# Kernel optimization log

Hardware: AMD Instinct MI355X
Metric: run time of the kernel (lower is better)

The kernel has to match this reference:

```python
import jax, jax.numpy as jnp
import numpy as np

N, E, D, H, ED = 50000, 400000, 64, 4, 16
C = D  # out_channels per head (GATv2Conv(model_dim, model_dim, ...))


def setup_inputs() -> dict:
    key = jax.random.key(0)
    ks = jax.random.split(key, 24)
    sD = 1.0 / np.sqrt(D)
    sE = 1.0 / np.sqrt(ED)
    sC = 1.0 / np.sqrt(C)
    inp = {
        "h": jax.random.normal(ks[0], (N, D), jnp.float32),
        "edge_index": jax.random.randint(ks[1], (2, E), 0, N, dtype=jnp.int32),
        "edge_attr": jax.random.normal(ks[2], (E, ED), jnp.float32),
    }
    for i, name in enumerate(["g1", "g2"]):
        b = 3 + i * 9
        inp[f"{name}_Wl"] = jax.random.normal(ks[b], (D, H * C), jnp.float32) * sD
        inp[f"{name}_bl"] = jax.random.normal(ks[b + 1], (H * C,), jnp.float32) * 0.02
        inp[f"{name}_Wr"] = jax.random.normal(ks[b + 2], (D, H * C), jnp.float32) * sD
        inp[f"{name}_br"] = jax.random.normal(ks[b + 3], (H * C,), jnp.float32) * 0.02
        inp[f"{name}_We"] = jax.random.normal(ks[b + 4], (ED, H * C), jnp.float32) * sE
        inp[f"{name}_att"] = jax.random.normal(ks[b + 5], (H, C), jnp.float32) * sC
        inp[f"{name}_bias"] = jax.random.normal(ks[b + 6], (C,), jnp.float32) * 0.02
        inp[f"ln{i+1}_g"] = jnp.ones((D,), jnp.float32)
        inp[f"ln{i+1}_b"] = jnp.zeros((D,), jnp.float32)
    return inp


def _layer_norm(x, g, b):
    mu = jnp.mean(x, axis=-1, keepdims=True)
    var = jnp.mean((x - mu) ** 2, axis=-1, keepdims=True)
    return (x - mu) * jax.lax.rsqrt(var + 1e-5) * g + b


def _gatv2(h, src, dst, edge_attr, Wl, bl, Wr, br, We, att, bias):
    # PyG GATv2Conv, concat=False, negative_slope=0.2, aggregation at dst
    xl = (h @ Wl + bl).reshape(N, H, C)  # source transform
    xr = (h @ Wr + br).reshape(N, H, C)  # target transform
    ez = (edge_attr @ We).reshape(E, H, C)
    x = jax.nn.leaky_relu(xl[src] + xr[dst] + ez, negative_slope=0.2)  # [E,H,C]
    alpha = jnp.einsum('ehc,hc->eh', x, att)  # attention logits per edge/head
    amax = jax.ops.segment_max(alpha, dst, num_segments=N)
    amax = jnp.where(jnp.isfinite(amax), amax, 0.0)
    ex = jnp.exp(alpha - amax[dst])
    denom = jax.ops.segment_sum(ex, dst, num_segments=N)
    a = ex / (denom[dst] + 1e-16)  # segment softmax over incoming edges
    out = jax.ops.segment_sum(xl[src] * a[..., None], dst, num_segments=N)  # [N,H,C]
    return jnp.mean(out, axis=1) + bias  # concat=False -> head mean, then bias


def reference(h, edge_index, edge_attr,
              g1_Wl, g1_bl, g1_Wr, g1_br, g1_We, g1_att, g1_bias, ln1_g, ln1_b,
              g2_Wl, g2_bl, g2_Wr, g2_br, g2_We, g2_att, g2_bias, ln2_g, ln2_b):
    src, dst = edge_index[0], edge_index[1]
    identity = h
    x = _gatv2(h, src, dst, edge_attr, g1_Wl, g1_bl, g1_Wr, g1_br, g1_We, g1_att, g1_bias)
    x = jax.nn.gelu(_layer_norm(x, ln1_g, ln1_b), approximate=False)
    x = _gatv2(x, src, dst, edge_attr, g2_Wl, g2_bl, g2_Wr, g2_br, g2_We, g2_att, g2_bias)
    x = _layer_norm(x, ln2_g, ln2_b)
    return jax.nn.gelu(x + identity, approximate=False)
```

## Files before the change

### kernel.cpp

```cpp
#include <hip/hip_runtime.h>
#include <math.h>

#define NN  50000
#define EE  400000
#define DD  64
#define HH  4
#define HC  256
#define EDD 16

__device__ __forceinline__ float gelu_exact(float x) {
    return 0.5f * x * (1.0f + erff(x * 0.70710678118654752440f));
}
__device__ __forceinline__ float fast_exp(float x) {
    return __builtin_amdgcn_exp2f(x * 1.44269504088896340736f);
}

__global__ void fill_u32(unsigned* __restrict__ p, unsigned v, int n) {
    int i = blockIdx.x * blockDim.x + threadIdx.x;
    int s = gridDim.x * blockDim.x;
    for (; i < n; i += s) p[i] = v;
}

__global__ void hist_k(const int* __restrict__ ei, int* __restrict__ deg) {
    int e = blockIdx.x * 256 + threadIdx.x;
    if (e < EE) atomicAdd(&deg[ei[EE + e]], 1);
}
__global__ void scan1_k(const int* __restrict__ deg, int* __restrict__ rowptr,
                        int* __restrict__ bsum) {
    __shared__ int s[256];
    int t = threadIdx.x, i = blockIdx.x * 256 + t;
    int v = (i < NN) ? deg[i] : 0;
    s[t] = v; __syncthreads();
    for (int o = 1; o < 256; o <<= 1) {
        int u = (t >= o) ? s[t - o] : 0;
        __syncthreads();
        s[t] += u;
        __syncthreads();
    }
    if (i < NN) rowptr[i] = s[t] - v;
    if (t == 255) bsum[blockIdx.x] = s[255];
}
__global__ void scan2_k(int* __restrict__ bsum, int nb) {
    __shared__ int s[256];
    int t = threadIdx.x;
    int v = (t < nb) ? bsum[t] : 0;
    s[t] = v; __syncthreads();
    for (int o = 1; o < 256; o <<= 1) {
        int u = (t >= o) ? s[t - o] : 0;
        __syncthreads();
        s[t] += u;
        __syncthreads();
    }
    if (t < nb) bsum[t] = s[t] - v;
}
__global__ void scan3_k(int* __restrict__ rowptr, const int* __restrict__ bsum,
                        int* __restrict__ cursor) {
    int i = blockIdx.x * 256 + threadIdx.x;
    if (i < NN) {
        int r = rowptr[i] + bsum[blockIdx.x];
        rowptr[i] = r;
        cursor[i] = r;
    }
    if (i == 0) rowptr[NN] = EE;
}
__global__ void scatter_k(const int* __restrict__ ei, int* __restrict__ cursor,
                          const float* __restrict__ ea,
                          int* __restrict__ srcs, float* __restrict__ ea_s) {
    int e = blockIdx.x * 256 + threadIdx.x;
    if (e >= EE) return;
    int dst = ei[EE + e];
    int pos = atomicAdd(&cursor[dst], 1);
    srcs[pos] = ei[e];
    const float4* s4 = (const float4*)(ea + (long)e * EDD);
    float4* d4 = (float4*)(ea_s + (long)pos * EDD);
    d4[0] = s4[0]; d4[1] = s4[1]; d4[2] = s4[2]; d4[3] = s4[3];
}

__global__ void wrange_k(const int* __restrict__ rowptr, int* __restrict__ wstart,
                         int nw, int cpe) {
    int w = blockIdx.x * 256 + threadIdx.x;
    if (w > nw) return;
    if (w == nw) { wstart[nw] = NN; return; }
    const int lo = w * cpe;
    int l = 0, r = NN;
    while (l < r) { int m = (l + r) >> 1; if (rowptr[m] >= lo) r = m; else l = m + 1; }
    wstart[w] = l;
}

__global__ __launch_bounds__(256) void gemm_node_lr(
    const float* __restrict__ X,
    const float* __restrict__ Wl, const float* __restrict__ bl,
    const float* __restrict__ Wr, const float* __restrict__ br,
    float* __restrict__ Yl, float* __restrict__ Yr)
{
    __shared__ float xs[32][64];
    const int tid  = threadIdx.x;
    const int col  = tid;
    const int base = blockIdx.x * 32;

#pragma unroll
    for (int i = 0; i < 2; i++) {
        const int f   = tid + i * 256;
        const int r   = f >> 4;
        const int row = base + r;
        const int rr  = (row < NN) ? row : (NN - 1);
        const float4 v = *(const float4*)(X + (long)rr * 64 + ((f & 15) << 2));
        *(float4*)&xs[r][(f & 15) << 2] = v;
    }

    float wl[64], wr[64];
#pragma unroll
    for (int k = 0; k < 64; k++) wl[k] = Wl[k * 256 + col];
#pragma unroll
    for (int k = 0; k < 64; k++) wr[k] = Wr[k * 256 + col];
    const float bbl = bl[col];
    const float bbr = br[col];

    __syncthreads();

#pragma unroll 2
    for (int r = 0; r < 32; r++) {
        const int row = base + r;
        float l0 = 0.f, l1 = 0.f, l2 = 0.f, l3 = 0.f;
        float r0 = 0.f, r1 = 0.f, r2 = 0.f, r3 = 0.f;
#pragma unroll
        for (int k4 = 0; k4 < 16; k4++) {
            const float4 xv = *(const float4*)&xs[r][k4 << 2];
            l0 = fmaf(xv.x, wl[k4 * 4],     l0);
            l1 = fmaf(xv.y, wl[k4 * 4 + 1], l1);
            l2 = fmaf(xv.z, wl[k4 * 4 + 2], l2);
            l3 = fmaf(xv.w, wl[k4 * 4 + 3], l3);
            r0 = fmaf(xv.x, wr[k4 * 4],     r0);
            r1 = fmaf(xv.y, wr[k4 * 4 + 1], r1);
            r2 = fmaf(xv.z, wr[k4 * 4 + 2], r2);
            r3 = fmaf(xv.w, wr[k4 * 4 + 3], r3);
        }
        if (row < NN) {
            Yl[(long)row * 256 + col] = (l0 + l1) + (l2 + l3) + bbl;
            Yr[(long)row * 256 + col] = (r0 + r1) + (r2 + r3) + bbr;
        }
    }
}

__global__ __launch_bounds__(256, 4) void fused_edge_node_k(
    const int* __restrict__ wstart,
    const int* __restrict__ rowptr, const int* __restrict__ srcs,
    const float* __restrict__ ea_s,
    const float* __restrict__ We, const float* __restrict__ att,
    const float* __restrict__ xl, const float* __restrict__ xr,
    const float* __restrict__ bias, const float* __restrict__ lng,
    const float* __restrict__ lnb, const float* __restrict__ identity,
    float* __restrict__ x1out, float* __restrict__ outp, int mode)
{
    const int lane = threadIdx.x & 63;
    const int h    = lane >> 4;
    const int jj   = lane & 15;
    const int gc   = (h << 6) + (jj << 2);
    const int cb   = jj << 2;

    float wreg[EDD][4];
#pragma unroll
    for (int k = 0; k < EDD; k++) {
        const float4 w4 = *(const float4*)(We + k * HC + gc);
        wreg[k][0] = w4.x; wreg[k][1] = w4.y; wreg[k][2] = w4.z; wreg[k][3] = w4.w;
    }
#pragma unroll
    for (int k = 0; k < EDD; k++)
#pragma unroll
        for (int j = 0; j < 4; j++) asm volatile("" : "+v"(wreg[k][j]));

    const float4 a4 = *(const float4*)(att + gc);

    const int wid  = blockIdx.x * 4 + (threadIdx.x >> 6);
    const int nbeg = __builtin_amdgcn_readfirstlane(wstart[wid]);
    const int nend = __builtin_amdgcn_readfirstlane(wstart[wid + 1]);

    int p0v = rowptr[nbeg];
    int p1v = rowptr[nbeg + 1];
    int sAn = srcs[p0v];
    int sBn = srcs[p0v + 1];

    for (int n = nbeg; n < nend; n++) {
        const int p0 = __builtin_amdgcn_readfirstlane(p0v);
        const int p1 = __builtin_amdgcn_readfirstlane(p1v);
        p0v = p1;
        p1v = rowptr[(n + 2 <= NN) ? (n + 2) : NN];
        int sA = sAn, sB = sBn;
        sAn = srcs[p1];
        sBn = srcs[p1 + 1];

        const float4 xrv = *(const float4*)(xr + (long)n * HC + gc);

        float dsum = 0.f;
        float ac0 = 0.f, ac1 = 0.f, ac2 = 0.f, ac3 = 0.f;

        int p = p0;
        for (; p + 1 < p1; p += 2) {
            const int srcA = __builtin_amdgcn_readfirstlane(sA);
            const int srcB = __builtin_amdgcn_readfirstlane(sB);
            sA = srcs[p + 2];
            sB = srcs[p + 3];

            const float4 xlvA = *(const float4*)(xl + (long)srcA * HC + gc);
            const float4 xlvB = *(const float4*)(xl + (long)srcB * HC + gc);

            const float4* __restrict__ e4 = (const float4*)(ea_s + (long)p * EDD);
            float eavA[EDD], eavB[EDD];
            *(float4*)&eavA[0]  = e4[0];
            *(float4*)&eavA[4]  = e4[1];
            *(float4*)&eavA[8]  = e4[2];
            *(float4*)&eavA[12] = e4[3];
            *(float4*)&eavB[0]  = e4[4];
            *(float4*)&eavB[4]  = e4[5];
            *(float4*)&eavB[8]  = e4[6];
            *(float4*)&eavB[12] = e4[7];

            float eA0 = 0.f, eA1 = 0.f, eA2 = 0.f, eA3 = 0.f;
            float eB0 = 0.f, eB1 = 0.f, eB2 = 0.f, eB3 = 0.f;
#pragma unroll
            for (int k = 0; k < EDD; k++) {
                eA0 = fmaf(eavA[k], wreg[k][0], eA0);
                eA1 = fmaf(eavA[k], wreg[k][1], eA1);
                eA2 = fmaf(eavA[k], wreg[k][2], eA2);
                eA3 = fmaf(eavA[k], wreg[k][3], eA3);
                eB0 = fmaf(eavB[k], wreg[k][0], eB0);
                eB1 = fmaf(eavB[k], wreg[k][1], eB1);
                eB2 = fmaf(eavB[k], wreg[k][2], eB2);
                eB3 = fmaf(eavB[k], wreg[k][3], eB3);
            }
            float sA0 = xlvA.x + xrv.x + eA0;
            float sA1 = xlvA.y + xrv.y + eA1;
            float sA2 = xlvA.z + xrv.z + eA2;
            float sA3 = xlvA.w + xrv.w + eA3;
            float sB0 = xlvB.x + xrv.x + eB0;
            float sB1 = xlvB.y + xrv.y + eB1;
            float sB2 = xlvB.z + xrv.z + eB2;
            float sB3 = xlvB.w + xrv.w + eB3;
            sA0 = (sA0 > 0.f) ? sA0 : 0.2f * sA0;
            sA1 = (sA1 > 0.f) ? sA1 : 0.2f * sA1;
            sA2 = (sA2 > 0.f) ? sA2 : 0.2f * sA2;
            sA3 = (sA3 > 0.f) ? sA3 : 0.2f * sA3;
            sB0 = (sB0 > 0.f) ? sB0 : 0.2f * sB0;
            sB1 = (sB1 > 0.f) ? sB1 : 0.2f * sB1;
            sB2 = (sB2 > 0.f) ? sB2 : 0.2f * sB2;
            sB3 = (sB3 > 0.f) ? sB3 : 0.2f * sB3;
            float pA = fmaf(sA0, a4.x, fmaf(sA1, a4.y, fmaf(sA2, a4.z, sA3 * a4.w)));
            float pB = fmaf(sB0, a4.x, fmaf(sB1, a4.y, fmaf(sB2, a4.z, sB3 * a4.w)));
            pA += __shfl_xor(pA, 1, 64);
            pB += __shfl_xor(pB, 1, 64);
            pA += __shfl_xor(pA, 2, 64);
            pB += __shfl_xor(pB, 2, 64);
            pA += __shfl_xor(pA, 4, 64);
            pB += __shfl_xor(pB, 4, 64);
            pA += __shfl_xor(pA, 8, 64);
            pB += __shfl_xor(pB, 8, 64);

            const float wA = fast_exp(pA);
            const float wB = fast_exp(pB);
            dsum += (wA + wB);
            ac0 = fmaf(wA, xlvA.x, ac0);
            ac1 = fmaf(wA, xlvA.y, ac1);
            ac2 = fmaf(wA, xlvA.z, ac2);
            ac3 = fmaf(wA, xlvA.w, ac3);
            ac0 = fmaf(wB, xlvB.x, ac0);
            ac1 = fmaf(wB, xlvB.y, ac1);
            ac2 = fmaf(wB, xlvB.z, ac2);
            ac3 = fmaf(wB, xlvB.w, ac3);
        }

        if (p < p1) {
            const int src = __builtin_amdgcn_readfirstlane(sA);
            const float4 xlv = *(const float4*)(xl + (long)src * HC + gc);
            const float4* __restrict__ e4 = (const float4*)(ea_s + (long)p * EDD);
            float eav[EDD];
            *(float4*)&eav[0]  = e4[0];
            *(float4*)&eav[4]  = e4[1];
            *(float4*)&eav[8]  = e4[2];
            *(float4*)&eav[12] = e4[3];
            float ez0 = 0.f, ez1 = 0.f, ez2 = 0.f, ez3 = 0.f;
#pragma unroll
            for (int k = 0; k < EDD; k++) {
                ez0 = fmaf(eav[k], wreg[k][0], ez0);
                ez1 = fmaf(eav[k], wreg[k][1], ez1);
                ez2 = fmaf(eav[k], wreg[k][2], ez2);
                ez3 = fmaf(eav[k], wreg[k][3], ez3);
            }
            float s0 = xlv.x + xrv.x + ez0;
            float s1 = xlv.y + xrv.y + ez1;
            float s2 = xlv.z + xrv.z + ez2;
            float s3 = xlv.w + xrv.w + ez3;
            s0 = (s0 > 0.f) ? s0 : 0.2f * s0;
            s1 = (s1 > 0.f) ? s1 : 0.2f * s1;
            s2 = (s2 > 0.f) ? s2 : 0.2f * s2;
            s3 = (s3 > 0.f) ? s3 : 0.2f * s3;
            float part = fmaf(s0, a4.x, fmaf(s1, a4.y, fmaf(s2, a4.z, s3 * a4.w)));
            part += __shfl_xor(part, 1, 64);
            part += __shfl_xor(part, 2, 64);
            part += __shfl_xor(part, 4, 64);
            part += __shfl_xor(part, 8, 64);
            const float w = fast_exp(part);
            dsum += w;
            ac0 = fmaf(w, xlv.x, ac0);
            ac1 = fmaf(w, xlv.y, ac1);
            ac2 = fmaf(w, xlv.z, ac2);
            ac3 = fmaf(w, xlv.w, ac3);
        }

        const float inv = 1.0f / (dsum + 1e-16f);
        float v0 = ac0 * inv, v1 = ac1 * inv, v2 = ac2 * inv, v3 = ac3 * inv;

        v0 += __shfl_xor(v0, 16, 64); v0 += __shfl_xor(v0, 32, 64);
        v1 += __shfl_xor(v1, 16, 64); v1 += __shfl_xor(v1, 32, 64);
        v2 += __shfl_xor(v2, 16, 64); v2 += __shfl_xor(v2, 32, 64);
        v3 += __shfl_xor(v3, 16, 64); v3 += __shfl_xor(v3, 32, 64);

        if (lane < 16) {
            const float4 b4 = *(const float4*)(bias + cb);
            v0 = v0 * 0.25f + b4.x;
            v1 = v1 * 0.25f + b4.y;
            v2 = v2 * 0.25f + b4.z;
            v3 = v3 * 0.25f + b4.w;

            float s = (v0 + v1) + (v2 + v3);
            s += __shfl_xor(s, 1, 64); s += __shfl_xor(s, 2, 64);
            s += __shfl_xor(s, 4, 64); s += __shfl_xor(s, 8, 64);
            const float mu = s * (1.0f / 64.0f);
            const float d0 = v0 - mu, d1 = v1 - mu, d2 = v2 - mu, d3 = v3 - mu;
            float q = (d0 * d0 + d1 * d1) + (d2 * d2 + d3 * d3);
            q += __shfl_xor(q, 1, 64); q += __shfl_xor(q, 2, 64);
            q += __shfl_xor(q, 4, 64); q += __shfl_xor(q, 8, 64);
            const float rs = rsqrtf(q * (1.0f / 64.0f) + 1e-5f);

            const float4 g4 = *(const float4*)(lng + cb);
            const float4 c4 = *(const float4*)(lnb + cb);
            float y0 = d0 * rs * g4.x + c4.x;
            float y1 = d1 * rs * g4.y + c4.y;
            float y2 = d2 * rs * g4.z + c4.z;
            float y3 = d3 * rs * g4.w + c4.w;

            if (mode == 0) {
                float4 o;
                o.x = gelu_exact(y0); o.y = gelu_exact(y1);
                o.z = gelu_exact(y2); o.w = gelu_exact(y3);
                *(float4*)(x1out + (long)n * DD + cb) = o;
            } else {
                const float4 id = *(const float4*)(identity + (long)n * DD + cb);
                float4 o;
                o.x = gelu_exact(y0 + id.x); o.y = gelu_exact(y1 + id.y);
                o.z = gelu_exact(y2 + id.z); o.w = gelu_exact(y3 + id.w);
                *(float4*)(outp + (long)n * DD + cb) = o;
            }
        }
    }
}

extern "C" void kernel_launch(void* const* d_in, const int* in_sizes, int n_in,
                              void* d_out, int out_size, void* d_ws, size_t ws_size,
                              hipStream_t stream) {
    (void)in_sizes; (void)n_in; (void)out_size; (void)ws_size;

    const float* h     = (const float*)d_in[0];
    const int*   ei    = (const int*)d_in[1];
    const float* ea    = (const float*)d_in[2];
    const float* g1Wl  = (const float*)d_in[3];
    const float* g1bl  = (const float*)d_in[4];
    const float* g1Wr  = (const float*)d_in[5];
    const float* g1br  = (const float*)d_in[6];
    const float* g1We  = (const float*)d_in[7];
    const float* g1att = (const float*)d_in[8];
    const float* g1bias= (const float*)d_in[9];
    const float* ln1g  = (const float*)d_in[10];
    const float* ln1b  = (const float*)d_in[11];
    const float* g2Wl  = (const float*)d_in[12];
    const float* g2bl  = (const float*)d_in[13];
    const float* g2Wr  = (const float*)d_in[14];
    const float* g2br  = (const float*)d_in[15];
    const float* g2We  = (const float*)d_in[16];
    const float* g2att = (const float*)d_in[17];
    const float* g2bias= (const float*)d_in[18];
    const float* ln2g  = (const float*)d_in[19];
    const float* ln2b  = (const float*)d_in[20];

    float* out = (float*)d_out;

    const int FUSED_BLOCKS = 4096;
    const int NW  = FUSED_BLOCKS * 4;
    const int CPE = (EE + NW - 1) / NW;

    float* ws = (float*)d_ws;
    size_t o = 0;
    float* xl     = ws + o;         o += 12800000;
    float* xr     = ws + o;         o += 12800000;
    float* x1     = ws + o;         o += 3200000;
    int*   rowptr = (int*)(ws + o); o += 50004;
    int*   deg    = (int*)(ws + o); o += 50000;
    int*   cursor = (int*)(ws + o); o += 50000;
    int*   bsum   = (int*)(ws + o); o += 256;
    int*   srcs   = (int*)(ws + o); o += 400016;
    int*   wstart = (int*)(ws + o); o += NW + 8;
    float* ea_s   = ws + o;         o += 6400000;

    const int GEMM_BLOCKS  = (NN + 31) / 32;
    const int SCAN_BLOCKS  = (NN + 255) / 256;
    const int EDGE_BLOCKS  = (EE + 255) / 256;
    const int WR_BLOCKS    = (NW + 1 + 255) / 256;

    fill_u32<<<256, 256, 0, stream>>>((unsigned*)deg, 0u, NN);
    hist_k<<<EDGE_BLOCKS, 256, 0, stream>>>(ei, deg);
    scan1_k<<<SCAN_BLOCKS, 256, 0, stream>>>(deg, rowptr, bsum);
    scan2_k<<<1, 256, 0, stream>>>(bsum, SCAN_BLOCKS);
    scan3_k<<<SCAN_BLOCKS, 256, 0, stream>>>(rowptr, bsum, cursor);
    wrange_k<<<WR_BLOCKS, 256, 0, stream>>>(rowptr, wstart, NW, CPE);
    scatter_k<<<EDGE_BLOCKS, 256, 0, stream>>>(ei, cursor, ea, srcs, ea_s);

    gemm_node_lr<<<GEMM_BLOCKS, 256, 0, stream>>>(h, g1Wl, g1bl, g1Wr, g1br, xl, xr);
    fused_edge_node_k<<<FUSED_BLOCKS, 256, 0, stream>>>(wstart, rowptr, srcs, ea_s,
                                                        g1We, g1att, xl, xr,
                                                        g1bias, ln1g, ln1b,
                                                        h, x1, out, 0);

    gemm_node_lr<<<GEMM_BLOCKS, 256, 0, stream>>>(x1, g2Wl, g2bl, g2Wr, g2br, xl, xr);
    fused_edge_node_k<<<FUSED_BLOCKS, 256, 0, stream>>>(wstart, rowptr, srcs, ea_s,
                                                        g2We, g2att, xl, xr,
                                                        g2bias, ln2g, ln2b,
                                                        h, x1, out, 1);
}
```

Baseline: 495.5 us.

## Unroll edge loop by four with masked tail, DPP reductions, full-wave LayerNorm epilogue

The per-node edge loop now handles four edges per iteration and replaces the remainder path with -INFINITY masking. It pads srcs and ea_s so the over-read past the last edge stays in bounds. Head reductions use DPP row adds instead of cross-lane shuffles. The LayerNorm/GELU epilogue is spread over all 64 lanes, one channel each, instead of 16 lanes handling float4. The aim is more memory-level parallelism and fewer shuffle and idle-lane costs, at the price of wasted work on nodes whose in-degree is not a multiple of four and higher register pressure.

After: 522.3 us. 5.4% more time.

```diff
diff --git a/kernel.cpp b/kernel.cpp
--- a/kernel.cpp
+++ b/kernel.cpp
@@ -13,6 +13,19 @@
 }
 __device__ __forceinline__ float fast_exp(float x) {
     return __builtin_amdgcn_exp2f(x * 1.44269504088896340736f);
+}
+
+template <int CTRL>
+__device__ __forceinline__ float dpp_add(float x) {
+    const int t = __builtin_amdgcn_update_dpp(0, __float_as_int(x), CTRL, 0xF, 0xF, true);
+    return x + __int_as_float(t);
+}
+__device__ __forceinline__ float row_sum16(float x) {
+    x = dpp_add<0x128>(x);
+    x = dpp_add<0x124>(x);
+    x = dpp_add<0x122>(x);
+    x = dpp_add<0x121>(x);
+    return x;
 }
 
 __global__ void fill_u32(unsigned* __restrict__ p, unsigned v, int n) {
@@ -77,8 +90,9 @@
 }
 
 __global__ void wrange_k(const int* __restrict__ rowptr, int* __restrict__ wstart,
-                         int nw, int cpe) {
+                         int* __restrict__ srcs, int nw, int cpe) {
     int w = blockIdx.x * 256 + threadIdx.x;
+    if (blockIdx.x == 0 && threadIdx.x < 16) srcs[EE + threadIdx.x] = 0;
     if (w > nw) return;
     if (w == nw) { wstart[nw] = NN; return; }
     const int lo = w * cpe;
@@ -142,6 +156,28 @@
     }
 }
 
+__device__ __forceinline__ float edge_part(const float ev[EDD], const float wreg[EDD][4],
+                                           const float4 xlv, const float4 xrv,
+                                           const float4 a4) {
+    float e0 = 0.f, e1 = 0.f, e2 = 0.f, e3 = 0.f;
+#pragma unroll
+    for (int k = 0; k < EDD; k++) {
+        e0 = fmaf(ev[k], wreg[k][0], e0);
+        e1 = fmaf(ev[k], wreg[k][1], e1);
+        e2 = fmaf(ev[k], wreg[k][2], e2);
+        e3 = fmaf(ev[k], wreg[k][3], e3);
+    }
+    float s0 = xlv.x + xrv.x + e0;
+    float s1 = xlv.y + xrv.y + e1;
+    float s2 = xlv.z + xrv.z + e2;
+    float s3 = xlv.w + xrv.w + e3;
+    s0 = (s0 > 0.f) ? s0 : 0.2f * s0;
+    s1 = (s1 > 0.f) ? s1 : 0.2f * s1;
+    s2 = (s2 > 0.f) ? s2 : 0.2f * s2;
+    s3 = (s3 > 0.f) ? s3 : 0.2f * s3;
+    return fmaf(s0, a4.x, fmaf(s1, a4.y, fmaf(s2, a4.z, s3 * a4.w)));
+}
+
 __global__ __launch_bounds__(256, 4) void fused_edge_node_k(
     const int* __restrict__ wstart,
     const int* __restrict__ rowptr, const int* __restrict__ srcs,
@@ -156,7 +192,7 @@
     const int h    = lane >> 4;
     const int jj   = lane & 15;
     const int gc   = (h << 6) + (jj << 2);
-    const int cb   = jj << 2;
+    const int c    = (jj << 2) + h;
 
     float wreg[EDD][4];
 #pragma unroll
@@ -170,6 +206,9 @@
         for (int j = 0; j < 4; j++) asm volatile("" : "+v"(wreg[k][j]));
 
     const float4 a4 = *(const float4*)(att + gc);
+    const float bb  = bias[c];
+    const float gg  = lng[c];
+    const float cc  = lnb[c];
 
     const int wid  = blockIdx.x * 4 + (threadIdx.x >> 6);
     const int nbeg = __builtin_amdgcn_readfirstlane(wstart[wid]);
@@ -177,134 +216,74 @@
 
     int p0v = rowptr[nbeg];
     int p1v = rowptr[nbeg + 1];
-    int sAn = srcs[p0v];
-    int sBn = srcs[p0v + 1];
+    int q0 = srcs[p0v], q1 = srcs[p0v + 1], q2 = srcs[p0v + 2], q3 = srcs[p0v + 3];
 
     for (int n = nbeg; n < nend; n++) {
         const int p0 = __builtin_amdgcn_readfirstlane(p0v);
         const int p1 = __builtin_amdgcn_readfirstlane(p1v);
         p0v = p1;
         p1v = rowptr[(n + 2 <= NN) ? (n + 2) : NN];
-        int sA = sAn, sB = sBn;
-        sAn = srcs[p1];
-        sBn = srcs[p1 + 1];
 
         const float4 xrv = *(const float4*)(xr + (long)n * HC + gc);
 
         float dsum = 0.f;
         float ac0 = 0.f, ac1 = 0.f, ac2 = 0.f, ac3 = 0.f;
 
-        int p = p0;
-        for (; p + 1 < p1; p += 2) {
-            const int srcA = __builtin_amdgcn_readfirstlane(sA);
-            const int srcB = __builtin_amdgcn_readfirstlane(sB);
-            sA = srcs[p + 2];
-            sB = srcs[p + 3];
-
-            const float4 xlvA = *(const float4*)(xl + (long)srcA * HC + gc);
-            const float4 xlvB = *(const float4*)(xl + (long)srcB * HC + gc);
+        for (int p = p0; p < p1; p += 4) {
+            const int s0 = __builtin_amdgcn_readfirstlane(q0);
+            const int s1 = __builtin_amdgcn_readfirstlane(q1);
+            const int s2 = __builtin_amdgcn_readfirstlane(q2);
+            const int s3 = __builtin_amdgcn_readfirstlane(q3);
+            q0 = srcs[p + 4]; q1 = srcs[p + 5];
+            q2 = srcs[p + 6]; q3 = srcs[p + 7];
+
+            const float4 x0 = *(const float4*)(xl + (long)s0 * HC + gc);
+            const float4 x1 = *(const float4*)(xl + (long)s1 * HC + gc);
+            const float4 x2 = *(const float4*)(xl + (long)s2 * HC + gc);
+            const float4 x3 = *(const float4*)(xl + (long)s3 * HC + gc);
 
             const float4* __restrict__ e4 = (const float4*)(ea_s + (long)p * EDD);
-            float eavA[EDD], eavB[EDD];
-            *(float4*)&eavA[0]  = e4[0];
-            *(float4*)&eavA[4]  = e4[1];
-            *(float4*)&eavA[8]  = e4[2];
-            *(float4*)&eavA[12] = e4[3];
-            *(float4*)&eavB[0]  = e4[4];
-            *(float4*)&eavB[4]  = e4[5];
-            *(float4*)&eavB[8]  = e4[6];
-            *(float4*)&eavB[12] = e4[7];
-
-            float eA0 = 0.f, eA1 = 0.f, eA2 = 0.f, eA3 = 0.f;
-            float eB0 = 0.f, eB1 = 0.f, eB2 = 0.f, eB3 = 0.f;
-#pragma unroll
-            for (int k = 0; k < EDD; k++) {
-                eA0 = fmaf(eavA[k], wreg[k][0], eA0);
-                eA1 = fmaf(eavA[k], wreg[k][1], eA1);
-                eA2 = fmaf(eavA[k], wreg[k][2], eA2);
-                eA3 = fmaf(eavA[k], wreg[k][3], eA3);
-                eB0 = fmaf(eavB[k], wreg[k][0], eB0);
-                eB1 = fmaf(eavB[k], wreg[k][1], eB1);
-                eB2 = fmaf(eavB[k], wreg[k][2], eB2);
-                eB3 = fmaf(eavB[k], wreg[k][3], eB3);
-            }
-            float sA0 = xlvA.x + xrv.x + eA0;
-            float sA1 = xlvA.y + xrv.y + eA1;
-            float sA2 = xlvA.z + xrv.z + eA2;
-            float sA3 = xlvA.w + xrv.w + eA3;
-            float sB0 = xlvB.x + xrv.x + eB0;
-            float sB1 = xlvB.y + xrv.y + eB1;
-            float sB2 = xlvB.z + xrv.z + eB2;
-            float sB3 = xlvB.w + xrv.w + eB3;
-            sA0 = (sA0 > 0.f) ? sA0 : 0.2f * sA0;
-            sA1 = (sA1 > 0.f) ? sA1 : 0.2f * sA1;
-            sA2 = (sA2 > 0.f) ? sA2 : 0.2f * sA2;
-            sA3 = (sA3 > 0.f) ? sA3 : 0.2f * sA3;
-            sB0 = (sB0 > 0.f) ? sB0 : 0.2f * sB0;
-            sB1 = (sB1 > 0.f) ? sB1 : 0.2f * sB1;
-            sB2 = (sB2 > 0.f) ? sB2 : 0.2f * sB2;
-            sB3 = (sB3 > 0.f) ? sB3 : 0.2f * sB3;
-            float pA = fmaf(sA0, a4.x, fmaf(sA1, a4.y, fmaf(sA2, a4.z, sA3 * a4.w)));
-            float pB = fmaf(sB0, a4.x, fmaf(sB1, a4.y, fmaf(sB2, a4.z, sB3 * a4.w)));
-            pA += __shfl_xor(pA, 1, 64);
-            pB += __shfl_xor(pB, 1, 64);
-            pA += __shfl_xor(pA, 2, 64);
-            pB += __shfl_xor(pB, 2, 64);
-            pA += __shfl_xor(pA, 4, 64);
-            pB += __shfl_xor(pB, 4, 64);
-            pA += __shfl_xor(pA, 8, 64);
-            pB += __shfl_xor(pB, 8, 64);
-
-            const float wA = fast_exp(pA);
-            const float wB = fast_exp(pB);
-            dsum += (wA + wB);
-            ac0 = fmaf(wA, xlvA.x, ac0);
-            ac1 = fmaf(wA, xlvA.y, ac1);
-            ac2 = fmaf(wA, xlvA.z, ac2);
-            ac3 = fmaf(wA, xlvA.w, ac3);
-            ac0 = fmaf(wB, xlvB.x, ac0);
-            ac1 = fmaf(wB, xlvB.y, ac1);
-            ac2 = fmaf(wB, xlvB.z, ac2);
-            ac3 = fmaf(wB, xlvB.w, ac3);
+            float ev0[EDD], ev1[EDD], ev2[EDD], ev3[EDD];
+            *(float4*)&ev0[0] = e4[0];  *(float4*)&ev0[4] = e4[1];
+            *(float4*)&ev0[8] = e4[2];  *(float4*)&ev0[12] = e4[3];
+            *(float4*)&ev1[0] = e4[4];  *(float4*)&ev1[4] = e4[5];
+            *(float4*)&ev1[8] = e4[6];  *(float4*)&ev1[12] = e4[7];
+            *(float4*)&ev2[0] = e4[8];  *(float4*)&ev2[4] = e4[9];
+            *(float4*)&ev2[8] = e4[10]; *(float4*)&ev2[12] = e4[11];
+            *(float4*)&ev3[0] = e4[12]; *(float4*)&ev3[4] = e4[13];
+            *(float4*)&ev3[8] = e4[14]; *(float4*)&ev3[12] = e4[15];
+
+            float pt0 = edge_part(ev0, wreg, x0, xrv, a4);
+            float pt1 = edge_part(ev1, wreg, x1, xrv, a4);
+            float pt2 = edge_part(ev2, wreg, x2, xrv, a4);
+            float pt3 = edge_part(ev3, wreg, x3, xrv, a4);
+
+            pt0 = row_sum16(pt0);
+            pt1 = row_sum16(pt1);
+            pt2 = row_sum16(pt2);
+            pt3 = row_sum16(pt3);
+
+            pt1 = (p + 1 < p1) ? pt1 : -INFINITY;
+            pt2 = (p + 2 < p1) ? pt2 : -INFINITY;
+            pt3 = (p + 3 < p1) ? pt3 : -INFINITY;
+
+            const float w0 = fast_exp(pt0);
+            const float w1 = fast_exp(pt1);
+            const float w2 = fast_exp(pt2);
+            const float w3 = fast_exp(pt3);
+            dsum += (w0 + w1) + (w2 + w3);
+            ac0 = fmaf(w0, x0.x, ac0); ac1 = fmaf(w0, x0.y, ac1);
+            ac2 = fmaf(w0, x0.z, ac2); ac3 = fmaf(w0, x0.w, ac3);
+            ac0 = fmaf(w1, x1.x, ac0); ac1 = fmaf(w1, x1.y, ac1);
+            ac2 = fmaf(w1, x1.z, ac2); ac3 = fmaf(w1, x1.w, ac3);
+            ac0 = fmaf(w2, x2.x, ac0); ac1 = fmaf(w2, x2.y, ac1);
+            ac2 = fmaf(w2, x2.z, ac2); ac3 = fmaf(w2, x2.w, ac3);
+            ac0 = fmaf(w3, x3.x, ac0); ac1 = fmaf(w3, x3.y, ac1);
+            ac2 = fmaf(w3, x3.z, ac2); ac3 = fmaf(w3, x3.w, ac3);
         }
 
-        if (p < p1) {
-            const int src = __builtin_amdgcn_readfirstlane(sA);
-            const float4 xlv = *(const float4*)(xl + (long)src * HC + gc);
-            const float4* __restrict__ e4 = (const float4*)(ea_s + (long)p * EDD);
-            float eav[EDD];
-            *(float4*)&eav[0]  = e4[0];
-            *(float4*)&eav[4]  = e4[1];
-            *(float4*)&eav[8]  = e4[2];
-            *(float4*)&eav[12] = e4[3];
-            float ez0 = 0.f, ez1 = 0.f, ez2 = 0.f, ez3 = 0.f;
-#pragma unroll
-            for (int k = 0; k < EDD; k++) {
-                ez0 = fmaf(eav[k], wreg[k][0], ez0);
-                ez1 = fmaf(eav[k], wreg[k][1], ez1);
-                ez2 = fmaf(eav[k], wreg[k][2], ez2);
-                ez3 = fmaf(eav[k], wreg[k][3], ez3);
-            }
-            float s0 = xlv.x + xrv.x + ez0;
-            float s1 = xlv.y + xrv.y + ez1;
-            float s2 = xlv.z + xrv.z + ez2;
-            float s3 = xlv.w + xrv.w + ez3;
-            s0 = (s0 > 0.f) ? s0 : 0.2f * s0;
-            s1 = (s1 > 0.f) ? s1 : 0.2f * s1;
-            s2 = (s2 > 0.f) ? s2 : 0.2f * s2;
-            s3 = (s3 > 0.f) ? s3 : 0.2f * s3;
-            float part = fmaf(s0, a4.x, fmaf(s1, a4.y, fmaf(s2, a4.z, s3 * a4.w)));
-            part += __shfl_xor(part, 1, 64);
-            part += __shfl_xor(part, 2, 64);
-            part += __shfl_xor(part, 4, 64);
-            part += __shfl_xor(part, 8, 64);
-            const float w = fast_exp(part);
-            dsum += w;
-            ac0 = fmaf(w, xlv.x, ac0);
-            ac1 = fmaf(w, xlv.y, ac1);
-            ac2 = fmaf(w, xlv.z, ac2);
-            ac3 = fmaf(w, xlv.w, ac3);
-        }
+        q0 = srcs[p1];     q1 = srcs[p1 + 1];
+        q2 = srcs[p1 + 2]; q3 = srcs[p1 + 3];
 
         const float inv = 1.0f / (dsum + 1e-16f);
         float v0 = ac0 * inv, v1 = ac1 * inv, v2 = ac2 * inv, v3 = ac3 * inv;
@@ -314,42 +293,23 @@
         v2 += __shfl_xor(v2, 16, 64); v2 += __shfl_xor(v2, 32, 64);
         v3 += __shfl_xor(v3, 16, 64); v3 += __shfl_xor(v3, 32, 64);
 
-        if (lane < 16) {
-            const float4 b4 = *(const float4*)(bias + cb);
-            v0 = v0 * 0.25f + b4.x;
-            v1 = v1 * 0.25f + b4.y;
-            v2 = v2 * 0.25f + b4.z;
-            v3 = v3 * 0.25f + b4.w;
-
-            float s = (v0 + v1) + (v2 + v3);
-            s += __shfl_xor(s, 1, 64); s += __shfl_xor(s, 2, 64);
-            s += __shfl_xor(s, 4, 64); s += __shfl_xor(s, 8, 64);
-            const float mu = s * (1.0f / 64.0f);
-            const float d0 = v0 - mu, d1 = v1 - mu, d2 = v2 - mu, d3 = v3 - mu;
-            float q = (d0 * d0 + d1 * d1) + (d2 * d2 + d3 * d3);
-            q += __shfl_xor(q, 1, 64); q += __shfl_xor(q, 2, 64);
-            q += __shfl_xor(q, 4, 64); q += __shfl_xor(q, 8, 64);
-            const float rs = rsqrtf(q * (1.0f / 64.0f) + 1e-5f);
-
-            const float4 g4 = *(const float4*)(lng + cb);
-            const float4 c4 = *(const float4*)(lnb + cb);
-            float y0 = d0 * rs * g4.x + c4.x;
-            float y1 = d1 * rs * g4.y + c4.y;
-            float y2 = d2 * rs * g4.z + c4.z;
-            float y3 = d3 * rs * g4.w + c4.w;
-
-            if (mode == 0) {
-                float4 o;
-                o.x = gelu_exact(y0); o.y = gelu_exact(y1);
-                o.z = gelu_exact(y2); o.w = gelu_exact(y3);
-                *(float4*)(x1out + (long)n * DD + cb) = o;
-            } else {
-                const float4 id = *(const float4*)(identity + (long)n * DD + cb);
-                float4 o;
-                o.x = gelu_exact(y0 + id.x); o.y = gelu_exact(y1 + id.y);
-                o.z = gelu_exact(y2 + id.z); o.w = gelu_exact(y3 + id.w);
-                *(float4*)(outp + (long)n * DD + cb) = o;
-            }
+        float vv = (h == 0) ? v0 : (h == 1) ? v1 : (h == 2) ? v2 : v3;
+        vv = vv * 0.25f + bb;
+
+        float s = row_sum16(vv);
+        s += __shfl_xor(s, 16, 64); s += __shfl_xor(s, 32, 64);
+        const float mu = s * (1.0f / 64.0f);
+        const float d  = vv - mu;
+        float qv = row_sum16(d * d);
+        qv += __shfl_xor(qv, 16, 64); qv += __shfl_xor(qv, 32, 64);
+        const float rs = rsqrtf(qv * (1.0f / 64.0f) + 1e-5f);
+
+        const float y = d * rs * gg + cc;
+        if (mode == 0) {
+            x1out[(long)n * DD + c] = gelu_exact(y);
+        } else {
+            const float id = identity[(long)n * DD + c];
+            outp[(long)n * DD + c] = gelu_exact(y + id);
         }
     }
 }
@@ -398,7 +358,7 @@
     int*   bsum   = (int*)(ws + o); o += 256;
     int*   srcs   = (int*)(ws + o); o += 400016;
     int*   wstart = (int*)(ws + o); o += NW + 8;
-    float* ea_s   = ws + o;         o += 6400000;
+    float* ea_s   = ws + o;         o += 6400064;
 
     const int GEMM_BLOCKS  = (NN + 31) / 32;
     const int SCAN_BLOCKS  = (NN + 255) / 256;
@@ -410,7 +370,7 @@
     scan1_k<<<SCAN_BLOCKS, 256, 0, stream>>>(deg, rowptr, bsum);
     scan2_k<<<1, 256, 0, stream>>>(bsum, SCAN_BLOCKS);
     scan3_k<<<SCAN_BLOCKS, 256, 0, stream>>>(rowptr, bsum, cursor);
-    wrange_k<<<WR_BLOCKS, 256, 0, stream>>>(rowptr, wstart, NW, CPE);
+    wrange_k<<<WR_BLOCKS, 256, 0, stream>>>(rowptr, wstart, srcs, NW, CPE);
     scatter_k<<<EDGE_BLOCKS, 256, 0, stream>>>(ei, cursor, ea, srcs, ea_s);
 
     gemm_node_lr<<<GEMM_BLOCKS, 256, 0, stream>>>(h, g1Wl, g1bl, g1Wr, g1br, xl, xr);
```
